# Kernel tuning notes

Measured on AMD Instinct MI355X. Metric: run time of the kernel, lower is better.

## Reference

```python
import jax, jax.numpy as jnp
import numpy as np

B, T, HORIZON = 64, 12, 12
N, E, K, H = 1024, 8, 3, 64
DIN, DOUT, YCOV = 1, 1, 1


def setup_inputs() -> dict:
    key = jax.random.key(0)
    ks = jax.random.split(key, 8)

    def xavier(k, shape):
        std = (2.0 / (shape[0] + shape[1])) ** 0.5
        return jax.random.normal(k, shape, jnp.float32) * std

    return {
        "x": jax.random.normal(ks[0], (B, T, N, DIN), jnp.float32),
        "y_cov": jax.random.normal(ks[1], (B, HORIZON, N, YCOV), jnp.float32),
        "node_embeddings": jax.random.normal(ks[2], (N, E), jnp.float32),
        "enc_gate_W": xavier(ks[3], (K * (DIN + H), 2 * H)),
        "enc_gate_b": jnp.zeros((2 * H,), jnp.float32),
        "enc_upd_W": xavier(ks[4], (K * (DIN + H), H)),
        "enc_upd_b": jnp.zeros((H,), jnp.float32),
        "dec_gate_W": xavier(ks[5], (K * (DOUT + YCOV + H), 2 * H)),
        "dec_gate_b": jnp.zeros((2 * H,), jnp.float32),
        "dec_upd_W": xavier(ks[6], (K * (DOUT + YCOV + H), H)),
        "dec_upd_b": jnp.zeros((H,), jnp.float32),
        "proj_W": xavier(ks[7], (H, DOUT)),
        "proj_b": jnp.zeros((DOUT,), jnp.float32),
    }


def _cheb(support, k):
    # Chebyshev polynomial set: T0=I, T1=A, Tk = 2*A@T_{k-1} - T_{k-2}
    mats = [jnp.eye(support.shape[0], dtype=support.dtype), support]
    for _ in range(2, k):
        mats.append(2.0 * (support @ mats[-1]) - mats[-2])
    return jnp.stack(mats)  # [K, N, N]


def _gcn(x, supports, W, b):
    # x: [B,N,C]; supports: [K,N,N] -> gather [B,N,K,C], concat k-major as in torch.cat
    xg = jnp.einsum('knm,bmc->bnkc', supports, x)
    Bb, Nn, Kk, Cc = xg.shape
    return xg.reshape(Bb, Nn, Kk * Cc) @ W + b


def _cell(x, state, supports, gW, gb, uW, ub):
    zr = jax.nn.sigmoid(_gcn(jnp.concatenate([x, state], axis=-1), supports, gW, gb))
    z, r = jnp.split(zr, 2, axis=-1)
    hc = jnp.tanh(_gcn(jnp.concatenate([x, z * state], axis=-1), supports, uW, ub))
    return r * state + (1.0 - r) * hc


def reference(x, y_cov, node_embeddings, enc_gate_W, enc_gate_b, enc_upd_W,
              enc_upd_b, dec_gate_W, dec_gate_b, dec_upd_W, dec_upd_b,
              proj_W, proj_b):
    # adaptive adjacency: softmax(relu(E E^T), axis=1)
    support = jax.nn.softmax(jax.nn.relu(node_embeddings @ node_embeddings.T), axis=1)
    supports = _cheb(support, K)

    # encoder over T_in steps (single rnn layer)
    h0 = jnp.zeros((x.shape[0], N, H), x.dtype)

    def enc_step(h, xt):
        h = _cell(xt, h, supports, enc_gate_W, enc_gate_b, enc_upd_W, enc_upd_b)
        return h, None

    h_t, _ = jax.lax.scan(enc_step, h0, jnp.swapaxes(x, 0, 1))

    go0 = jnp.zeros((x.shape[0], N, DOUT), x.dtype)

    def dec_step(carry, yt):
        go, h = carry
        h = _cell(jnp.concatenate([go, yt], axis=-1), h, supports,
                  dec_gate_W, dec_gate_b, dec_upd_W, dec_upd_b)
        go = h @ proj_W + proj_b
        return (go, h), go

    _, outs = jax.lax.scan(dec_step, (go0, h_t), jnp.swapaxes(y_cov, 0, 1))
    return jnp.swapaxes(outs, 0, 1)  # [B, horizon, N, output_dim]
```

## Files before the change

### kernel.cpp

```cpp
#include <hip/hip_runtime.h>


typedef __attribute__((ext_vector_type(8))) short bf16x8;
typedef __attribute__((ext_vector_type(4))) float f32x4;
typedef __attribute__((ext_vector_type(4))) unsigned short u16x4;

__device__ __forceinline__ float b2f(unsigned short u) {
    union { unsigned int i; float f; } v; v.i = ((unsigned int)u) << 16; return v.f;
}
__device__ __forceinline__ unsigned short f2b(float f) {
    union { float f; unsigned int i; } v; v.f = f;
    unsigned int r = v.i + 0x7FFFu + ((v.i >> 16) & 1u);
    return (unsigned short)(r >> 16);
}

__global__ __launch_bounds__(256) void gemm_bt(
    const unsigned short* __restrict__ P, int lda,
    const unsigned short* __restrict__ QT, int ldb,
    unsigned short* __restrict__ C, int ldc,
    int K, float scale)
{
    __shared__ __align__(16) unsigned short As[128 * 32];
    __shared__ __align__(16) unsigned short Bs[128 * 32];
    const int tid = threadIdx.x;
    const int m0 = blockIdx.y << 7, n0 = blockIdx.x << 7;
    const int w = tid >> 6, l = tid & 63;
    const int wm = (w >> 1) << 6, wn = (w & 1) << 6;
    const int lr = l & 15, lq = l >> 4;
    const int arow = tid >> 2, ak = (tid & 3) << 3;
    f32x4 acc[4][4] = {};

    for (int k0 = 0; k0 < K; k0 += 32) {
        bf16x8 ta[2], tb[2];
#pragma unroll
        for (int p = 0; p < 2; ++p)
            ta[p] = *(const bf16x8*)(P + (size_t)(m0 + arow + (p << 6)) * lda + k0 + ak);
#pragma unroll
        for (int p = 0; p < 2; ++p)
            tb[p] = *(const bf16x8*)(QT + (size_t)(n0 + arow + (p << 6)) * ldb + k0 + ak);
#pragma unroll
        for (int p = 0; p < 2; ++p) {
            *(bf16x8*)&As[((arow + (p << 6)) << 5) + ak] = ta[p];
            *(bf16x8*)&Bs[((arow + (p << 6)) << 5) + ak] = tb[p];
        }
        __syncthreads();
        bf16x8 a[4], b[4];
#pragma unroll
        for (int i = 0; i < 4; ++i)
            a[i] = *(const bf16x8*)&As[((wm + (i << 4) + lr) << 5) + (lq << 3)];
#pragma unroll
        for (int j = 0; j < 4; ++j)
            b[j] = *(const bf16x8*)&Bs[((wn + (j << 4) + lr) << 5) + (lq << 3)];
#pragma unroll
        for (int i = 0; i < 4; ++i)
#pragma unroll
            for (int j = 0; j < 4; ++j)
                acc[i][j] = __builtin_amdgcn_mfma_f32_16x16x32_bf16(a[i], b[j], acc[i][j], 0, 0, 0);
        __syncthreads();
    }
#pragma unroll
    for (int i = 0; i < 4; ++i)
#pragma unroll
        for (int j = 0; j < 4; ++j)
#pragma unroll
            for (int r = 0; r < 4; ++r) {
                const int m = m0 + wm + (i << 4) + (lq << 2) + r;
                const int n = n0 + wn + (j << 4) + lr;
                C[(size_t)m * ldc + n] = f2b(acc[i][j][r] * scale);
            }
}

__global__ __launch_bounds__(256) void gru_gate(
    const unsigned short* __restrict__ Hb, const unsigned short* __restrict__ S, int ldS,
    const unsigned short* __restrict__ WT, const float* __restrict__ bias,
    const float* __restrict__ wx, const float* __restrict__ xin, int t,
    const unsigned short* __restrict__ XSgT, int xsrow, const unsigned short* __restrict__ Go,
    const float* __restrict__ H32,
    unsigned short* __restrict__ Zb, unsigned short* __restrict__ ZhT, float* __restrict__ R,
    int dec)
{
    __shared__ __align__(16) unsigned short As[128 * 32];
    __shared__ __align__(16) unsigned short Bs[128 * 32];
    const int tid = threadIdx.x;
    const int rb = blockIdx.x;
    const int b = rb >> 3, n0 = (rb & 7) << 7;
    const int w = tid >> 6, l = tid & 63;
    const int wm = (w >> 1) << 6, wn = (w & 1) << 6;
    const int lr = l & 15, lq = l >> 4;
    const int arow = tid >> 2, ak = (tid & 3) << 3;
    f32x4 acc[4][4] = {};

    const unsigned short* sbase[3];
    size_t sstride[3];
    sbase[0] = Hb + ((size_t)(b << 10) + n0) * 64;        sstride[0] = 64;
    sbase[1] = S + (size_t)n0 * ldS + (b << 6);           sstride[1] = (size_t)ldS;
    sbase[2] = S + (size_t)(1024 + n0) * ldS + (b << 6);  sstride[2] = (size_t)ldS;

    for (int kk0 = 0; kk0 < 192; kk0 += 32) {
        const int seg = kk0 >> 6, so = kk0 & 63;
        bf16x8 ta[2], tb[2];
#pragma unroll
        for (int p = 0; p < 2; ++p)
            ta[p] = *(const bf16x8*)(sbase[seg] + (size_t)(arow + (p << 6)) * sstride[seg] + so + ak);
#pragma unroll
        for (int p = 0; p < 2; ++p)
            tb[p] = *(const bf16x8*)(WT + (size_t)(arow + (p << 6)) * 192 + kk0 + ak);
#pragma unroll
        for (int p = 0; p < 2; ++p) {
            *(bf16x8*)&As[((arow + (p << 6)) << 5) + ak] = ta[p];
            *(bf16x8*)&Bs[((arow + (p << 6)) << 5) + ak] = tb[p];
        }
        __syncthreads();
        bf16x8 a[4], bb[4];
#pragma unroll
        for (int i = 0; i < 4; ++i)
            a[i] = *(const bf16x8*)&As[((wm + (i << 4) + lr) << 5) + (lq << 3)];
#pragma unroll
        for (int j = 0; j < 4; ++j)
            bb[j] = *(const bf16x8*)&Bs[((wn + (j << 4) + lr) << 5) + (lq << 3)];
#pragma unroll
        for (int i = 0; i < 4; ++i)
#pragma unroll
            for (int j = 0; j < 4; ++j)
                acc[i][j] = __builtin_amdgcn_mfma_f32_16x16x32_bf16(a[i], bb[j], acc[i][j], 0, 0, 0);
        __syncthreads();
    }

#pragma unroll
    for (int i = 0; i < 4; ++i) {
        const int node_base = n0 + wm + (i << 4) + (lq << 2);
        float c0[4], c1[4], c2[4], c3[4], c4[4], c5[4];
        for (int r = 0; r < 4; ++r) {
            const int node = node_base + r;
            if (!dec) {
                c0[r] = xin[((b * 12 + t) << 10) + node];
                c1[r] = b2f(XSgT[(size_t)(xsrow + t * 64 + b) * 2048 + node]);
                c2[r] = b2f(XSgT[(size_t)(xsrow + t * 64 + b) * 2048 + 1024 + node]);
                c3[r] = c4[r] = c5[r] = 0.f;
            } else {
                c0[r] = b2f(Go[(b << 10) + node]);
                c1[r] = xin[((b * 12 + t) << 10) + node];
                c2[r] = b2f(S[(size_t)node * ldS + 4096 + b]);
                c3[r] = b2f(XSgT[(size_t)(xsrow + t * 64 + b) * 2048 + node]);
                c4[r] = b2f(S[(size_t)(1024 + node) * ldS + 4096 + b]);
                c5[r] = b2f(XSgT[(size_t)(xsrow + t * 64 + b) * 2048 + 1024 + node]);
            }
        }
#pragma unroll
        for (int j = 0; j < 4; ++j) {
            const int jc = wn + (j << 4) + lr;
            const float bj = bias[jc];
            const float w0 = wx[jc], w1 = wx[128 + jc], w2 = wx[256 + jc];
            float w3 = 0.f, w4 = 0.f, w5 = 0.f;
            if (dec) { w3 = wx[384 + jc]; w4 = wx[512 + jc]; w5 = wx[640 + jc]; }
            if (jc < 64) {
                u16x4 pack;
                for (int r = 0; r < 4; ++r) {
                    float v = acc[i][j][r] + bj + c0[r] * w0 + c1[r] * w1 + c2[r] * w2
                              + c3[r] * w3 + c4[r] * w4 + c5[r] * w5;
                    float g = 1.f / (1.f + __expf(-v));
                    const int node = node_base + r;
                    const size_t idx = ((size_t)(b << 10) + node) * 64 + jc;
                    float zh = g * H32[idx];
                    unsigned short zb = f2b(zh);
                    Zb[idx] = zb;
                    pack[r] = zb;
                }
                *(u16x4*)&ZhT[(size_t)((b << 6) + jc) * 1024 + node_base] = pack;
            } else {
                for (int r = 0; r < 4; ++r) {
                    float v = acc[i][j][r] + bj + c0[r] * w0 + c1[r] * w1 + c2[r] * w2
                              + c3[r] * w3 + c4[r] * w4 + c5[r] * w5;
                    float g = 1.f / (1.f + __expf(-v));
                    const int node = node_base + r;
                    R[((size_t)(b << 10) + node) * 64 + (jc - 64)] = g;
                }
            }
        }
    }
}

__global__ __launch_bounds__(256) void gru_update(
    const unsigned short* __restrict__ Zb, const unsigned short* __restrict__ S, int ldS,
    const unsigned short* __restrict__ WT, const float* __restrict__ bias,
    const float* __restrict__ wx, const float* __restrict__ xin, int t,
    const unsigned short* __restrict__ XSgT, int xsrow, const unsigned short* __restrict__ Go,
    const float* __restrict__ Rg,
    float* __restrict__ H32, unsigned short* __restrict__ Hb, unsigned short* __restrict__ XhT,
    int dec)
{
    __shared__ __align__(16) unsigned short As[128 * 32];
    __shared__ __align__(16) unsigned short Bs[64 * 32];
    const int tid = threadIdx.x;
    const int rb = blockIdx.x;
    const int b = rb >> 3, n0 = (rb & 7) << 7;
    const int w = tid >> 6, l = tid & 63;
    const int wm = w << 5;
    const int lr = l & 15, lq = l >> 4;
    const int arow = tid >> 2, ak = (tid & 3) << 3;
    f32x4 acc[2][4] = {};

    const unsigned short* sbase[3];
    size_t sstride[3];
    sbase[0] = Zb + ((size_t)(b << 10) + n0) * 64;        sstride[0] = 64;
    sbase[1] = S + (size_t)n0 * ldS + (b << 6);           sstride[1] = (size_t)ldS;
    sbase[2] = S + (size_t)(1024 + n0) * ldS + (b << 6);  sstride[2] = (size_t)ldS;

    for (int kk0 = 0; kk0 < 192; kk0 += 32) {
        const int seg = kk0 >> 6, so = kk0 & 63;
        bf16x8 ta[2], tb;
#pragma unroll
        for (int p = 0; p < 2; ++p)
            ta[p] = *(const bf16x8*)(sbase[seg] + (size_t)(arow + (p << 6)) * sstride[seg] + so + ak);
        tb = *(const bf16x8*)(WT + (size_t)arow * 192 + kk0 + ak);
#pragma unroll
        for (int p = 0; p < 2; ++p)
            *(bf16x8*)&As[((arow + (p << 6)) << 5) + ak] = ta[p];
        if (arow < 64) *(bf16x8*)&Bs[(arow << 5) + ak] = tb;
        __syncthreads();
        bf16x8 a[2], bb[4];
#pragma unroll
        for (int i = 0; i < 2; ++i)
            a[i] = *(const bf16x8*)&As[((wm + (i << 4) + lr) << 5) + (lq << 3)];
#pragma unroll
        for (int j = 0; j < 4; ++j)
            bb[j] = *(const bf16x8*)&Bs[(((j << 4) + lr) << 5) + (lq << 3)];
#pragma unroll
        for (int i = 0; i < 2; ++i)
#pragma unroll
            for (int j = 0; j < 4; ++j)
                acc[i][j] = __builtin_amdgcn_mfma_f32_16x16x32_bf16(a[i], bb[j], acc[i][j], 0, 0, 0);
        __syncthreads();
    }

#pragma unroll
    for (int i = 0; i < 2; ++i) {
        const int node_base = n0 + wm + (i << 4) + (lq << 2);
        float c0[4], c1[4], c2[4], c3[4], c4[4], c5[4];
        for (int r = 0; r < 4; ++r) {
            const int node = node_base + r;
            if (!dec) {
                c0[r] = xin[((b * 12 + t) << 10) + node];
                c1[r] = b2f(XSgT[(size_t)(xsrow + t * 64 + b) * 2048 + node]);
                c2[r] = b2f(XSgT[(size_t)(xsrow + t * 64 + b) * 2048 + 1024 + node]);
                c3[r] = c4[r] = c5[r] = 0.f;
            } else {
                c0[r] = b2f(Go[(b << 10) + node]);
                c1[r] = xin[((b * 12 + t) << 10) + node];
                c2[r] = b2f(S[(size_t)node * ldS + 4096 + b]);
                c3[r] = b2f(XSgT[(size_t)(xsrow + t * 64 + b) * 2048 + node]);
                c4[r] = b2f(S[(size_t)(1024 + node) * ldS + 4096 + b]);
                c5[r] = b2f(XSgT[(size_t)(xsrow + t * 64 + b) * 2048 + 1024 + node]);
            }
        }
#pragma unroll
        for (int j = 0; j < 4; ++j) {
            const int jc = (j << 4) + lr;
            const float bj = bias[jc];
            const float w0 = wx[jc], w1 = wx[64 + jc], w2 = wx[128 + jc];
            float w3 = 0.f, w4 = 0.f, w5 = 0.f;
            if (dec) { w3 = wx[192 + jc]; w4 = wx[256 + jc]; w5 = wx[320 + jc]; }
            u16x4 pack;
            for (int r = 0; r < 4; ++r) {
                float v = acc[i][j][r] + bj + c0[r] * w0 + c1[r] * w1 + c2[r] * w2
                          + c3[r] * w3 + c4[r] * w4 + c5[r] * w5;
                float hc = tanhf(v);
                const int node = node_base + r;
                const size_t idx = ((size_t)(b << 10) + node) * 64 + jc;
                float rr = Rg[idx];
                float hn = rr * H32[idx] + (1.f - rr) * hc;
                H32[idx] = hn;
                unsigned short hb = f2b(hn);
                Hb[idx] = hb;
                pack[r] = hb;
            }
            *(u16x4*)&XhT[(size_t)((b << 6) + jc) * 1024 + node_base] = pack;
        }
    }
}

__global__ __launch_bounds__(256) void adj_softmax(
    const float* __restrict__ E, unsigned short* __restrict__ A)
{
    __shared__ float Es[8192];
    __shared__ float vals[1024];
    __shared__ float red[8];
    const int tid = threadIdx.x;
    const int r = blockIdx.x;
    for (int i = tid; i < 8192; i += 256) Es[i] = E[i];
    __syncthreads();
    float er[8];
#pragma unroll
    for (int e = 0; e < 8; ++e) er[e] = Es[(r << 3) + e];
    float lmax = -1e30f;
    for (int c = tid; c < 1024; c += 256) {
        float s = 0.f;
#pragma unroll
        for (int e = 0; e < 8; ++e) s += er[e] * Es[(c << 3) + e];
        s = fmaxf(s, 0.f);
        vals[c] = s;
        lmax = fmaxf(lmax, s);
    }
    for (int off = 32; off; off >>= 1) lmax = fmaxf(lmax, __shfl_down(lmax, off, 64));
    if ((tid & 63) == 0) red[tid >> 6] = lmax;
    __syncthreads();
    const float m = fmaxf(fmaxf(red[0], red[1]), fmaxf(red[2], red[3]));
    float lsum = 0.f;
    for (int c = tid; c < 1024; c += 256) {
        float e = __expf(vals[c] - m);
        vals[c] = e;
        lsum += e;
    }
    for (int off = 32; off; off >>= 1) lsum += __shfl_down(lsum, off, 64);
    if ((tid & 63) == 0) red[4 + (tid >> 6)] = lsum;
    __syncthreads();
    const float inv = 1.f / (red[4] + red[5] + red[6] + red[7]);
    for (int c = tid; c < 1024; c += 256)
        A[(r << 10) + c] = f2b(vals[c] * inv);
}

__global__ __launch_bounds__(256) void transpose_bf16(
    const unsigned short* __restrict__ src, unsigned short* __restrict__ dst)
{
    __shared__ unsigned short tile[64][65];
    const int bx = blockIdx.x & 15, by = blockIdx.x >> 4;
    const int x0 = bx << 6, y0 = by << 6;
    for (int i = threadIdx.x; i < 4096; i += 256) {
        const int r = i >> 6, c = i & 63;
        tile[r][c] = src[((y0 + r) << 10) + x0 + c];
    }
    __syncthreads();
    for (int i = threadIdx.x; i < 4096; i += 256) {
        const int r = i >> 6, c = i & 63;
        dst[((x0 + r) << 10) + y0 + c] = tile[c][r];
    }
}

__global__ __launch_bounds__(256) void build_xall(
    const float* __restrict__ x, const float* __restrict__ y,
    unsigned short* __restrict__ XallT)
{
    const int id = blockIdx.x * 256 + threadIdx.x;
    const int row = id >> 10, n = id & 1023;
    int t, b;
    const float* src;
    if (row < 768) { t = row >> 6; b = row & 63; src = x; }
    else { const int rr = row - 768; t = rr >> 6; b = rr & 63; src = y; }
    XallT[id] = f2b(src[((b * 12 + t) << 10) + n]);
}

__global__ __launch_bounds__(256) void wprep(
    const float* egW, const float* egb,
    const float* euW, const float* eub,
    const float* dgW, const float* dgb,
    const float* duW, const float* dub,
    const float* pW, const float* pb,
    unsigned short* WgTe, unsigned short* WuTe, unsigned short* WgTd, unsigned short* WuTd,
    float* wxge, float* wxue, float* wxgd, float* wxud,
    float* bge, float* bue, float* bgd, float* bud,
    float* projW, float* projb)
{
    const int tid = threadIdx.x;
    for (int i = tid; i < 128 * 192; i += 256) {
        const int j = i / 192, kk = i % 192, k = kk >> 6, c = kk & 63;
        float v = egW[(k * 65 + 1 + c) * 128 + j];
        if (k == 0) v -= egW[(131 + c) * 128 + j];
        WgTe[i] = f2b(v);
    }
    for (int i = tid; i < 64 * 192; i += 256) {
        const int j = i / 192, kk = i % 192, k = kk >> 6, c = kk & 63;
        float v = euW[(k * 65 + 1 + c) * 64 + j];
        if (k == 0) v -= euW[(131 + c) * 64 + j];
        WuTe[i] = f2b(v);
    }
    for (int i = tid; i < 128 * 192; i += 256) {
        const int j = i / 192, kk = i % 192, k = kk >> 6, c = kk & 63;
        float v = dgW[(k * 66 + 2 + c) * 128 + j];
        if (k == 0) v -= dgW[(134 + c) * 128 + j];
        WgTd[i] = f2b(v);
    }
    for (int i = tid; i < 64 * 192; i += 256) {
        const int j = i / 192, kk = i % 192, k = kk >> 6, c = kk & 63;
        float v = duW[(k * 66 + 2 + c) * 64 + j];
        if (k == 0) v -= duW[(134 + c) * 64 + j];
        WuTd[i] = f2b(v);
    }
    for (int i = tid; i < 384; i += 256) {
        const int k = i >> 7, j = i & 127;
        float v;
        if (k == 0) v = egW[j] - egW[130 * 128 + j];
        else if (k == 1) v = egW[65 * 128 + j];
        else v = egW[130 * 128 + j];
        wxge[i] = v;
    }
    for (int i = tid; i < 192; i += 256) {
        const int k = i >> 6, j = i & 63;
        float v;
        if (k == 0) v = euW[j] - euW[130 * 64 + j];
        else if (k == 1) v = euW[65 * 64 + j];
        else v = euW[130 * 64 + j];
        wxue[i] = v;
    }
    for (int i = tid; i < 768; i += 256) {
        const int k = i >> 7, j = i & 127;
        float v;
        switch (k) {
            case 0: v = dgW[j] - dgW[132 * 128 + j]; break;
            case 1: v = dgW[128 + j] - dgW[133 * 128 + j]; break;
            case 2: v = dgW[66 * 128 + j]; break;
            case 3: v = dgW[67 * 128 + j]; break;
            case 4: v = dgW[132 * 128 + j]; break;
            default: v = dgW[133 * 128 + j]; break;
        }
        wxgd[i] = v;
    }
    for (int i = tid; i < 384; i += 256) {
        const int k = i >> 6, j = i & 63;
        float v;
        switch (k) {
            case 0: v = duW[j] - duW[132 * 64 + j]; break;
            case 1: v = duW[64 + j] - duW[133 * 64 + j]; break;
            case 2: v = duW[66 * 64 + j]; break;
            case 3: v = duW[67 * 64 + j]; break;
            case 4: v = duW[132 * 64 + j]; break;
            default: v = duW[133 * 64 + j]; break;
        }
        wxud[i] = v;
    }
    for (int i = tid; i < 128; i += 256) bge[i] = egb[i];
    for (int i = tid; i < 64; i += 256) bue[i] = eub[i];
    for (int i = tid; i < 128; i += 256) bgd[i] = dgb[i];
    for (int i = tid; i < 64; i += 256) bud[i] = dub[i];
    for (int i = tid; i < 64; i += 256) projW[i] = pW[i];
    if (tid == 0) projb[0] = pb[0];
}

__global__ __launch_bounds__(256) void proj_kernel(
    const float* __restrict__ H32, const float* __restrict__ projW, const float* __restrict__ projb,
    unsigned short* __restrict__ Go, unsigned short* __restrict__ XhT,
    float* __restrict__ out, int t)
{
    const int w = threadIdx.x >> 6, l = threadIdx.x & 63;
    const int row = (blockIdx.x << 2) + w;
    float v = H32[((size_t)row << 6) + l] * projW[l];
#pragma unroll
    for (int off = 32; off; off >>= 1) v += __shfl_down(v, off, 64);
    if (l == 0) {
        const float go = v + projb[0];
        const unsigned short gb = f2b(go);
        const int b = row >> 10, n = row & 1023;
        Go[row] = gb;
        XhT[((size_t)(4096 + b) << 10) + n] = gb;
        out[((size_t)(b * 12 + t) << 10) + n] = go;
    }
}

extern "C" void kernel_launch(void* const* d_in, const int* in_sizes, int n_in,
                              void* d_out, int out_size, void* d_ws, size_t ws_size,
                              hipStream_t stream)
{
    (void)in_sizes; (void)n_in; (void)out_size; (void)ws_size;
    const float* x    = (const float*)d_in[0];
    const float* ycov = (const float*)d_in[1];
    const float* E    = (const float*)d_in[2];
    const float* egW  = (const float*)d_in[3];
    const float* egb  = (const float*)d_in[4];
    const float* euW  = (const float*)d_in[5];
    const float* eub  = (const float*)d_in[6];
    const float* dgW  = (const float*)d_in[7];
    const float* dgb  = (const float*)d_in[8];
    const float* duW  = (const float*)d_in[9];
    const float* dub  = (const float*)d_in[10];
    const float* pW   = (const float*)d_in[11];
    const float* pb   = (const float*)d_in[12];
    float* out = (float*)d_out;

    size_t off = 0;
    auto carve = [&](size_t bytes) -> void* {
        void* p = (char*)d_ws + off;
        off += (bytes + 255) & ~(size_t)255;
        return p;
    };
    unsigned short* AA    = (unsigned short*)carve(2048ull * 1024 * 2);
    unsigned short* XSgT  = (unsigned short*)carve(1536ull * 2048 * 2);
    unsigned short* XhT   = (unsigned short*)carve(4224ull * 1024 * 2);
    unsigned short* ZhT   = (unsigned short*)carve(4096ull * 1024 * 2);
    unsigned short* S     = (unsigned short*)carve(2048ull * 4224 * 2);
    unsigned short* Hb    = (unsigned short*)carve(65536ull * 64 * 2);
    float*          H32   = (float*)carve(65536ull * 64 * 4);
    unsigned short* Zb    = (unsigned short*)carve(65536ull * 64 * 2);
    float*          R     = (float*)carve(65536ull * 64 * 4);
    unsigned short* Go    = (unsigned short*)carve(65536ull * 2);
    unsigned short* WgTe  = (unsigned short*)carve(128ull * 192 * 2);
    unsigned short* WuTe  = (unsigned short*)carve(64ull * 192 * 2);
    unsigned short* WgTd  = (unsigned short*)carve(128ull * 192 * 2);
    unsigned short* WuTd  = (unsigned short*)carve(64ull * 192 * 2);
    float* wxge = (float*)carve(384 * 4);
    float* wxue = (float*)carve(192 * 4);
    float* wxgd = (float*)carve(768 * 4);
    float* wxud = (float*)carve(384 * 4);
    float* bge  = (float*)carve(128 * 4);
    float* bue  = (float*)carve(64 * 4);
    float* bgd  = (float*)carve(128 * 4);
    float* bud  = (float*)carve(64 * 4);
    float* prW  = (float*)carve(64 * 4);
    float* prb  = (float*)carve(4);
    unsigned short* AT    = Zb;
    unsigned short* XallT = Zb + 1024ull * 1024;

    hipMemsetAsync(XhT, 0, 4224ull * 1024 * 2, stream);
    hipMemsetAsync(Hb, 0, 65536ull * 64 * 2, stream);
    hipMemsetAsync(H32, 0, 65536ull * 64 * 4, stream);
    hipMemsetAsync(Go, 0, 65536ull * 2, stream);

    adj_softmax<<<1024, 256, 0, stream>>>(E, AA);
    transpose_bf16<<<256, 256, 0, stream>>>(AA, AT);
    gemm_bt<<<dim3(8, 8), 256, 0, stream>>>(AA, 1024, AT, 1024, AA + 1024 * 1024, 1024, 1024, 2.0f);
    build_xall<<<6144, 256, 0, stream>>>(x, ycov, XallT);
    gemm_bt<<<dim3(16, 12), 256, 0, stream>>>(XallT, 1024, AA, 1024, XSgT, 2048, 1024, 1.0f);
    wprep<<<1, 256, 0, stream>>>(egW, egb, euW, eub, dgW, dgb, duW, dub, pW, pb,
                                 WgTe, WuTe, WgTd, WuTd, wxge, wxue, wxgd, wxud,
                                 bge, bue, bgd, bud, prW, prb);

    for (int t = 0; t < 12; ++t) {
        gemm_bt<<<dim3(32, 16), 256, 0, stream>>>(AA, 1024, XhT, 1024, S, 4224, 1024, 1.0f);
        gru_gate<<<512, 256, 0, stream>>>(Hb, S, 4224, WgTe, bge, wxge, x, t, XSgT, 0, Go, H32,
                                          Zb, ZhT, R, 0);
        gemm_bt<<<dim3(32, 16), 256, 0, stream>>>(AA, 1024, ZhT, 1024, S, 4224, 1024, 1.0f);
        gru_update<<<512, 256, 0, stream>>>(Zb, S, 4224, WuTe, bue, wxue, x, t, XSgT, 0, Go,
                                            R, H32, Hb, XhT, 0);
    }
    for (int t = 0; t < 12; ++t) {
        gemm_bt<<<dim3(33, 16), 256, 0, stream>>>(AA, 1024, XhT, 1024, S, 4224, 1024, 1.0f);
        gru_gate<<<512, 256, 0, stream>>>(Hb, S, 4224, WgTd, bgd, wxgd, ycov, t, XSgT, 768, Go, H32,
                                          Zb, ZhT, R, 1);
        gemm_bt<<<dim3(32, 16), 256, 0, stream>>>(AA, 1024, ZhT, 1024, S, 4224, 1024, 1.0f);
        gru_update<<<512, 256, 0, stream>>>(Zb, S, 4224, WuTd, bud, wxud, ycov, t, XSgT, 768, Go,
                                            R, H32, Hb, XhT, 1);
        proj_kernel<<<16384, 256, 0, stream>>>(H32, prW, prb, Go, XhT, out, t);
    }
}
```

Before: 3.047 ms.

## Load GEMM tiles directly to LDS, fuse decoder projection, parallelize weight prep

The GEMM-style kernels now use global_load_lds to move 16-byte chunks from global memory straight into shared memory, instead of staging them through registers. The decoder's output projection is folded into the gru_update epilogue: a 16-lane shuffle reduction produces Go and the output directly, which removes the separate proj_kernel launch and its re-read of H32. The weight-prep kernel is also spread over 64 blocks instead of one. The trade-offs are reliance on the direct-to-LDS load path and extra shuffle work and registers in the update kernel.

```diff
diff --git a/kernel.cpp b/kernel.cpp
--- a/kernel.cpp
+++ b/kernel.cpp
@@ -13,6 +13,10 @@
     unsigned int r = v.i + 0x7FFFu + ((v.i >> 16) & 1u);
     return (unsigned short)(r >> 16);
 }
+
+#define GLOAD_LDS16(g, l) __builtin_amdgcn_global_load_lds( \
+    (const __attribute__((address_space(1))) void*)(g),     \
+    (__attribute__((address_space(3))) void*)(l), 16, 0, 0)
 
 __global__ __launch_bounds__(256) void gemm_bt(
     const unsigned short* __restrict__ P, int lda,
@@ -31,18 +35,14 @@
     f32x4 acc[4][4] = {};
 
     for (int k0 = 0; k0 < K; k0 += 32) {
-        bf16x8 ta[2], tb[2];
 #pragma unroll
         for (int p = 0; p < 2; ++p)
-            ta[p] = *(const bf16x8*)(P + (size_t)(m0 + arow + (p << 6)) * lda + k0 + ak);
+            GLOAD_LDS16(P + (size_t)(m0 + arow + (p << 6)) * lda + k0 + ak,
+                        &As[((arow + (p << 6)) << 5) + ak]);
 #pragma unroll
         for (int p = 0; p < 2; ++p)
-            tb[p] = *(const bf16x8*)(QT + (size_t)(n0 + arow + (p << 6)) * ldb + k0 + ak);
-#pragma unroll
-        for (int p = 0; p < 2; ++p) {
-            *(bf16x8*)&As[((arow + (p << 6)) << 5) + ak] = ta[p];
-            *(bf16x8*)&Bs[((arow + (p << 6)) << 5) + ak] = tb[p];
-        }
+            GLOAD_LDS16(QT + (size_t)(n0 + arow + (p << 6)) * ldb + k0 + ak,
+                        &Bs[((arow + (p << 6)) << 5) + ak]);
         __syncthreads();
         bf16x8 a[4], b[4];
 #pragma unroll
@@ -98,18 +98,14 @@
 
     for (int kk0 = 0; kk0 < 192; kk0 += 32) {
         const int seg = kk0 >> 6, so = kk0 & 63;
-        bf16x8 ta[2], tb[2];
 #pragma unroll
         for (int p = 0; p < 2; ++p)
-            ta[p] = *(const bf16x8*)(sbase[seg] + (size_t)(arow + (p << 6)) * sstride[seg] + so + ak);
+            GLOAD_LDS16(sbase[seg] + (size_t)(arow + (p << 6)) * sstride[seg] + so + ak,
+                        &As[((arow + (p << 6)) << 5) + ak]);
 #pragma unroll
         for (int p = 0; p < 2; ++p)
-            tb[p] = *(const bf16x8*)(WT + (size_t)(arow + (p << 6)) * 192 + kk0 + ak);
-#pragma unroll
-        for (int p = 0; p < 2; ++p) {
-            *(bf16x8*)&As[((arow + (p << 6)) << 5) + ak] = ta[p];
-            *(bf16x8*)&Bs[((arow + (p << 6)) << 5) + ak] = tb[p];
-        }
+            GLOAD_LDS16(WT + (size_t)(arow + (p << 6)) * 192 + kk0 + ak,
+                        &Bs[((arow + (p << 6)) << 5) + ak]);
         __syncthreads();
         bf16x8 a[4], bb[4];
 #pragma unroll
@@ -187,6 +183,8 @@
     const unsigned short* __restrict__ XSgT, int xsrow, const unsigned short* __restrict__ Go,
     const float* __restrict__ Rg,
     float* __restrict__ H32, unsigned short* __restrict__ Hb, unsigned short* __restrict__ XhT,
+    const float* __restrict__ prW, const float* __restrict__ prb,
+    unsigned short* __restrict__ GoOut, float* __restrict__ outp,
     int dec)
 {
     __shared__ __align__(16) unsigned short As[128 * 32];
@@ -208,15 +206,11 @@
 
     for (int kk0 = 0; kk0 < 192; kk0 += 32) {
         const int seg = kk0 >> 6, so = kk0 & 63;
-        bf16x8 ta[2], tb;
 #pragma unroll
         for (int p = 0; p < 2; ++p)
-            ta[p] = *(const bf16x8*)(sbase[seg] + (size_t)(arow + (p << 6)) * sstride[seg] + so + ak);
-        tb = *(const bf16x8*)(WT + (size_t)arow * 192 + kk0 + ak);
-#pragma unroll
-        for (int p = 0; p < 2; ++p)
-            *(bf16x8*)&As[((arow + (p << 6)) << 5) + ak] = ta[p];
-        if (arow < 64) *(bf16x8*)&Bs[(arow << 5) + ak] = tb;
+            GLOAD_LDS16(sbase[seg] + (size_t)(arow + (p << 6)) * sstride[seg] + so + ak,
+                        &As[((arow + (p << 6)) << 5) + ak]);
+        GLOAD_LDS16(WT + (size_t)arow * 192 + kk0 + ak, &Bs[(arow << 5) + ak]);
         __syncthreads();
         bf16x8 a[2], bb[4];
 #pragma unroll
@@ -231,6 +225,12 @@
             for (int j = 0; j < 4; ++j)
                 acc[i][j] = __builtin_amdgcn_mfma_f32_16x16x32_bf16(a[i], bb[j], acc[i][j], 0, 0, 0);
         __syncthreads();
+    }
+
+    float pw[4];
+    if (dec) {
+#pragma unroll
+        for (int j = 0; j < 4; ++j) pw[j] = prW[(j << 4) + lr];
     }
 
 #pragma unroll
@@ -253,6 +253,7 @@
                 c5[r] = b2f(XSgT[(size_t)(xsrow + t * 64 + b) * 2048 + 1024 + node]);
             }
         }
+        float psum[4] = {0.f, 0.f, 0.f, 0.f};
 #pragma unroll
         for (int j = 0; j < 4; ++j) {
             const int jc = (j << 4) + lr;
@@ -273,8 +274,26 @@
                 unsigned short hb = f2b(hn);
                 Hb[idx] = hb;
                 pack[r] = hb;
+                if (dec) psum[r] += hn * pw[j];
             }
             *(u16x4*)&XhT[(size_t)((b << 6) + jc) * 1024 + node_base] = pack;
+        }
+        if (dec) {
+#pragma unroll
+            for (int r = 0; r < 4; ++r) {
+                float v = psum[r];
+                v += __shfl_down(v, 8, 16);
+                v += __shfl_down(v, 4, 16);
+                v += __shfl_down(v, 2, 16);
+                v += __shfl_down(v, 1, 16);
+                if (lr == 0) {
+                    const int node = node_base + r;
+                    const float go = v + prb[0];
+                    GoOut[(b << 10) + node] = f2b(go);
+                    XhT[((size_t)(4096 + b) << 10) + node] = f2b(go);
+                    outp[((size_t)(b * 12 + t) << 10) + node] = go;
+                }
+            }
         }
     }
 }
@@ -360,32 +379,33 @@
     float* bge, float* bue, float* bgd, float* bud,
     float* projW, float* projb)
 {
-    const int tid = threadIdx.x;
-    for (int i = tid; i < 128 * 192; i += 256) {
+    const int tid0 = blockIdx.x * 256 + threadIdx.x;
+    const int stride = 256 * gridDim.x;
+    for (int i = tid0; i < 128 * 192; i += stride) {
         const int j = i / 192, kk = i % 192, k = kk >> 6, c = kk & 63;
         float v = egW[(k * 65 + 1 + c) * 128 + j];
         if (k == 0) v -= egW[(131 + c) * 128 + j];
         WgTe[i] = f2b(v);
     }
-    for (int i = tid; i < 64 * 192; i += 256) {
+    for (int i = tid0; i < 64 * 192; i += stride) {
         const int j = i / 192, kk = i % 192, k = kk >> 6, c = kk & 63;
         float v = euW[(k * 65 + 1 + c) * 64 + j];
         if (k == 0) v -= euW[(131 + c) * 64 + j];
         WuTe[i] = f2b(v);
     }
-    for (int i = tid; i < 128 * 192; i += 256) {
+    for (int i = tid0; i < 128 * 192; i += stride) {
         const int j = i / 192, kk = i % 192, k = kk >> 6, c = kk & 63;
         float v = dgW[(k * 66 + 2 + c) * 128 + j];
         if (k == 0) v -= dgW[(134 + c) * 128 + j];
         WgTd[i] = f2b(v);
     }
-    for (int i = tid; i < 64 * 192; i += 256) {
+    for (int i = tid0; i < 64 * 192; i += stride) {
         const int j = i / 192, kk = i % 192, k = kk >> 6, c = kk & 63;
         float v = duW[(k * 66 + 2 + c) * 64 + j];
         if (k == 0) v -= duW[(134 + c) * 64 + j];
         WuTd[i] = f2b(v);
     }
-    for (int i = tid; i < 384; i += 256) {
+    for (int i = tid0; i < 384; i += stride) {
         const int k = i >> 7, j = i & 127;
         float v;
         if (k == 0) v = egW[j] - egW[130 * 128 + j];
@@ -393,7 +413,7 @@
         else v = egW[130 * 128 + j];
         wxge[i] = v;
     }
-    for (int i = tid; i < 192; i += 256) {
+    for (int i = tid0; i < 192; i += stride) {
         const int k = i >> 6, j = i & 63;
         float v;
         if (k == 0) v = euW[j] - euW[130 * 64 + j];
@@ -401,7 +421,7 @@
         else v = euW[130 * 64 + j];
         wxue[i] = v;
     }
-    for (int i = tid; i < 768; i += 256) {
+    for (int i = tid0; i < 768; i += stride) {
         const int k = i >> 7, j = i & 127;
         float v;
         switch (k) {
@@ -414,7 +434,7 @@
         }
         wxgd[i] = v;
     }
-    for (int i = tid; i < 384; i += 256) {
+    for (int i = tid0; i < 384; i += stride) {
         const int k = i >> 6, j = i & 63;
         float v;
         switch (k) {
@@ -427,32 +447,12 @@
         }
         wxud[i] = v;
     }
-    for (int i = tid; i < 128; i += 256) bge[i] = egb[i];
-    for (int i = tid; i < 64; i += 256) bue[i] = eub[i];
-    for (int i = tid; i < 128; i += 256) bgd[i] = dgb[i];
-    for (int i = tid; i < 64; i += 256) bud[i] = dub[i];
-    for (int i = tid; i < 64; i += 256) projW[i] = pW[i];
-    if (tid == 0) projb[0] = pb[0];
-}
-
-__global__ __launch_bounds__(256) void proj_kernel(
-    const float* __restrict__ H32, const float* __restrict__ projW, const float* __restrict__ projb,
-    unsigned short* __restrict__ Go, unsigned short* __restrict__ XhT,
-    float* __restrict__ out, int t)
-{
-    const int w = threadIdx.x >> 6, l = threadIdx.x & 63;
-    const int row = (blockIdx.x << 2) + w;
-    float v = H32[((size_t)row << 6) + l] * projW[l];
-#pragma unroll
-    for (int off = 32; off; off >>= 1) v += __shfl_down(v, off, 64);
-    if (l == 0) {
-        const float go = v + projb[0];
-        const unsigned short gb = f2b(go);
-        const int b = row >> 10, n = row & 1023;
-        Go[row] = gb;
-        XhT[((size_t)(4096 + b) << 10) + n] = gb;
-        out[((size_t)(b * 12 + t) << 10) + n] = go;
-    }
+    for (int i = tid0; i < 128; i += stride) bge[i] = egb[i];
+    for (int i = tid0; i < 64; i += stride) bue[i] = eub[i];
+    for (int i = tid0; i < 128; i += stride) bgd[i] = dgb[i];
+    for (int i = tid0; i < 64; i += stride) bud[i] = dub[i];
+    for (int i = tid0; i < 64; i += stride) projW[i] = pW[i];
+    if (tid0 == 0) projb[0] = pb[0];
 }
 
 extern "C" void kernel_launch(void* const* d_in, const int* in_sizes, int n_in,
@@ -518,9 +518,9 @@
     gemm_bt<<<dim3(8, 8), 256, 0, stream>>>(AA, 1024, AT, 1024, AA + 1024 * 1024, 1024, 1024, 2.0f);
     build_xall<<<6144, 256, 0, stream>>>(x, ycov, XallT);
     gemm_bt<<<dim3(16, 12), 256, 0, stream>>>(XallT, 1024, AA, 1024, XSgT, 2048, 1024, 1.0f);
-    wprep<<<1, 256, 0, stream>>>(egW, egb, euW, eub, dgW, dgb, duW, dub, pW, pb,
-                                 WgTe, WuTe, WgTd, WuTd, wxge, wxue, wxgd, wxud,
-                                 bge, bue, bgd, bud, prW, prb);
+    wprep<<<64, 256, 0, stream>>>(egW, egb, euW, eub, dgW, dgb, duW, dub, pW, pb,
+                                  WgTe, WuTe, WgTd, WuTd, wxge, wxue, wxgd, wxud,
+                                  bge, bue, bgd, bud, prW, prb);
 
     for (int t = 0; t < 12; ++t) {
         gemm_bt<<<dim3(32, 16), 256, 0, stream>>>(AA, 1024, XhT, 1024, S, 4224, 1024, 1.0f);
@@ -528,7 +528,7 @@
                                           Zb, ZhT, R, 0);
         gemm_bt<<<dim3(32, 16), 256, 0, stream>>>(AA, 1024, ZhT, 1024, S, 4224, 1024, 1.0f);
         gru_update<<<512, 256, 0, stream>>>(Zb, S, 4224, WuTe, bue, wxue, x, t, XSgT, 0, Go,
-                                            R, H32, Hb, XhT, 0);
+                                            R, H32, Hb, XhT, prW, prb, Go, out, 0);
     }
     for (int t = 0; t < 12; ++t) {
         gemm_bt<<<dim3(33, 16), 256, 0, stream>>>(AA, 1024, XhT, 1024, S, 4224, 1024, 1.0f);
@@ -536,7 +536,6 @@
                                           Zb, ZhT, R, 1);
         gemm_bt<<<dim3(32, 16), 256, 0, stream>>>(AA, 1024, ZhT, 1024, S, 4224, 1024, 1.0f);
         gru_update<<<512, 256, 0, stream>>>(Zb, S, 4224, WuTd, bud, wxud, ycov, t, XSgT, 768, Go,
-                                            R, H32, Hb, XhT, 1);
-        proj_kernel<<<16384, 256, 0, stream>>>(H32, prW, prb, Go, XhT, out, t);
-    }
-}
+                                            R, H32, Hb, XhT, prW, prb, Go, out, 1);
+    }
+}
```

New measurement: 2.737 ms. 10.2% less time.
